# Performance work log

Measured on AMD Instinct MI355X. Metric: run time of the kernel, lower is better.

## Reference

```python
import jax, jax.numpy as jnp
import numpy as np

NUM_NODES = 1_000_000
H, OUT, R, B = 128, 64, 64, 8
N0, N1, N2 = 262144, 16384, 1024
E0, E1 = 409600, 20480


def setup_inputs() -> dict:
    key = jax.random.key(0)
    ks = jax.random.split(key, 16)
    return {
        'src_ids': jax.random.randint(ks[0], (N0,), 0, NUM_NODES, dtype=jnp.int32),
        'e0_src':  jax.random.randint(ks[1], (E0,), 0, N0, dtype=jnp.int32),
        'e0_dst':  jax.random.randint(ks[2], (E0,), 0, N1, dtype=jnp.int32),
        'e0_type': jax.random.randint(ks[3], (E0,), 0, R, dtype=jnp.int32),
        'norm0':   jax.random.uniform(ks[4], (E0,), dtype=jnp.float32),
        'e1_src':  jax.random.randint(ks[5], (E1,), 0, N1, dtype=jnp.int32),
        'e1_dst':  jax.random.randint(ks[6], (E1,), 0, N2, dtype=jnp.int32),
        'e1_type': jax.random.randint(ks[7], (E1,), 0, R, dtype=jnp.int32),
        'norm1':   jax.random.uniform(ks[8], (E1,), dtype=jnp.float32),
        'emb':   jax.random.normal(ks[9], (NUM_NODES, H), dtype=jnp.float32) * 0.02,
        'V1':    jax.random.normal(ks[10], (B, H, H), dtype=jnp.float32) / np.float32(np.sqrt(H)),
        'comp1': jax.random.normal(ks[11], (R, B), dtype=jnp.float32) / np.float32(np.sqrt(B)),
        'b1':    jnp.zeros((H,), jnp.float32),
        'V2':    jax.random.normal(ks[12], (B, H, OUT), dtype=jnp.float32) / np.float32(np.sqrt(H)),
        'comp2': jax.random.normal(ks[13], (R, B), dtype=jnp.float32) / np.float32(np.sqrt(B)),
        'b2':    jnp.zeros((OUT,), jnp.float32),
    }


def rel_graph_conv(x, src, dst, etype, norm, V, comp, bias, n_dst):
    """Basis-decomposed relational graph conv (no self loop).

    W_r = sum_b comp[r, b] * V[b];  m_e = (x[src_e] @ W_{etype_e}) * norm_e
    out[v] = sum_{e: dst_e = v} m_e + bias
    """
    h_src = x[src]                              # [E, in] gather
    c = comp[etype]                             # [E, B] per-edge basis coeffs
    m = jnp.zeros((h_src.shape[0], V.shape[2]), x.dtype)
    for b in range(V.shape[0]):                 # small fixed loop over bases
        m = m + c[:, b:b + 1] * (h_src @ V[b])  # [E, out]
    m = m * norm[:, None]
    out = jax.ops.segment_sum(m, dst, num_segments=n_dst)  # scatter-add
    return out + bias


def reference(src_ids, e0_src, e0_dst, e0_type, norm0,
              e1_src, e1_dst, e1_type, norm1,
              emb, V1, comp1, b1, V2, comp2, b2):
    x = emb[src_ids]                                                   # [N0, H] embedding lookup
    h = jax.nn.relu(rel_graph_conv(x, e0_src, e0_dst, e0_type, norm0,
                                   V1, comp1, b1, N1))                 # [N1, H]
    out = rel_graph_conv(h, e1_src, e1_dst, e1_type, norm1,
                         V2, comp2, b2, N2)                            # [N2, OUT]
    return out
```

## Files before the change

kernel.cpp:

```cpp
#include <hip/hip_runtime.h>

#define N0 262144
#define N1 16384
#define N2 1024
#define E0 409600
#define E1 20480
#define HD 128
#define PACK1 131072
#define PACK2 65536
#define BCAP 64
#define PREP_BLOCKS 2448

typedef __attribute__((ext_vector_type(8))) __bf16 bf16x8;
typedef __attribute__((ext_vector_type(4))) float f32x4;

__device__ __forceinline__ unsigned short f2bf(float f) {
    unsigned int u = __builtin_bit_cast(unsigned int, f);
    u += 0x7fffu + ((u >> 16) & 1u);
    return (unsigned short)(u >> 16);
}
__device__ __forceinline__ float bf2f(unsigned short h) {
    unsigned int u = ((unsigned int)h) << 16;
    return __builtin_bit_cast(float, u);
}

__global__ __launch_bounds__(256) void prep_k(const float* __restrict__ V1,
                                              unsigned short* __restrict__ V1p,
                                              const float* __restrict__ V2,
                                              unsigned short* __restrict__ V2p,
                                              const int* __restrict__ src_ids,
                                              const int* __restrict__ e0s,
                                              const int* __restrict__ e0d,
                                              const int* __restrict__ e0t,
                                              const float* __restrict__ n0,
                                              int* __restrict__ cnt0,
                                              int2* __restrict__ rec0,
                                              const int* __restrict__ e1s,
                                              const int* __restrict__ e1d,
                                              const int* __restrict__ e1t,
                                              const float* __restrict__ n1,
                                              int* __restrict__ cnt1,
                                              int2* __restrict__ rec1) {
    int idx = blockIdx.x * 256 + threadIdx.x;
    if (idx < PACK1 + PACK2) {
        const float* V = idx < PACK1 ? V1 : V2;
        unsigned short* o = idx < PACK1 ? V1p : V2p;
        int NT = idx < PACK1 ? 8 : 4;
        int q = idx < PACK1 ? idx : idx - PACK1;
        int i  = q & 7;
        int l  = (q >> 3) & 63;
        int kt = (q >> 9) & 31;
        int nt = q >> 14;
        int k = kt * 32 + (l >> 4) * 8 + i;
        int j = nt * 16 + (l & 15);
        o[q] = f2bf(V[(size_t)k * (NT * 16) + j]);
    } else if (idx < PACK1 + PACK2 + E0) {
        int e = idx - (PACK1 + PACK2);
        int d = e0d[e];
        int slot = atomicAdd(&cnt0[d], 1);
        if (slot < BCAP)
            rec0[(size_t)d * BCAP + slot] =
                make_int2(src_ids[e0s[e]] | (e0t[e] << 24),
                          __builtin_bit_cast(int, n0[e]));
    } else {
        int e = idx - (PACK1 + PACK2 + E0);
        int d = e1d[e];
        int slot = atomicAdd(&cnt1[d], 1);
        if (slot < BCAP)
            rec1[(size_t)d * BCAP + slot] =
                make_int2(e1s[e] | (e1t[e] << 24),
                          __builtin_bit_cast(int, n1[e]));
    }
}

template <bool L0>
__device__ __forceinline__ void agg_bucket8(const int2* __restrict__ bucket, int n,
                                            const float* __restrict__ compS,
                                            const float* __restrict__ xf,
                                            const unsigned short* __restrict__ xh,
                                            int lane, float* acc) {
#pragma unroll
    for (int i = 0; i < 16; i++) acc[i] = 0.f;
    if (n <= 0) return;
    const int last = n - 1;

    auto ldx = [&](int2 r) -> float2 {
        int s = r.x & 0xFFFFFF;
        if constexpr (L0) {
            return *(const float2*)(xf + (size_t)s * HD + lane * 2);
        } else {
            unsigned int u = *(const unsigned int*)(xh + (size_t)s * HD + lane * 2);
            return make_float2(bf2f((unsigned short)(u & 0xffffu)),
                               bf2f((unsigned short)(u >> 16)));
        }
    };
    auto consume = [&](int2 r, float2 x, bool valid) {
        float nrm = valid ? __builtin_bit_cast(float, r.y) : 0.f;
        const float* cp = compS + ((unsigned)r.x >> 24) * 8;
        float4 c0 = *(const float4*)cp;
        float4 c1 = *(const float4*)(cp + 4);
        float xx = x.x * nrm, xy = x.y * nrm;
        acc[0]  += c0.x * xx; acc[1]  += c0.x * xy;
        acc[2]  += c0.y * xx; acc[3]  += c0.y * xy;
        acc[4]  += c0.z * xx; acc[5]  += c0.z * xy;
        acc[6]  += c0.w * xx; acc[7]  += c0.w * xy;
        acc[8]  += c1.x * xx; acc[9]  += c1.x * xy;
        acc[10] += c1.y * xx; acc[11] += c1.y * xy;
        acc[12] += c1.z * xx; acc[13] += c1.z * xy;
        acc[14] += c1.w * xx; acc[15] += c1.w * xy;
    };

    for (int e = 0; e <= last; e += 8) {
        int2 r0 = bucket[e];
        int2 r1 = bucket[e + 1 <= last ? e + 1 : last];
        int2 r2 = bucket[e + 2 <= last ? e + 2 : last];
        int2 r3 = bucket[e + 3 <= last ? e + 3 : last];
        int2 r4 = bucket[e + 4 <= last ? e + 4 : last];
        int2 r5 = bucket[e + 5 <= last ? e + 5 : last];
        int2 r6 = bucket[e + 6 <= last ? e + 6 : last];
        int2 r7 = bucket[e + 7 <= last ? e + 7 : last];
        float2 x0 = ldx(r0);
        float2 x1 = ldx(r1);
        float2 x2 = ldx(r2);
        float2 x3 = ldx(r3);
        float2 x4 = ldx(r4);
        float2 x5 = ldx(r5);
        float2 x6 = ldx(r6);
        float2 x7 = ldx(r7);
        consume(r0, x0, true);
        consume(r1, x1, e + 1 <= last);
        consume(r2, x2, e + 2 <= last);
        consume(r3, x3, e + 3 <= last);
        consume(r4, x4, e + 4 <= last);
        consume(r5, x5, e + 5 <= last);
        consume(r6, x6, e + 6 <= last);
        consume(r7, x7, e + 7 <= last);
    }
}

__device__ __forceinline__ void write_lds_row(unsigned short* aT, int v, int lane,
                                              const float* acc) {
#pragma unroll
    for (int b = 0; b < 8; b++) {
        unsigned int o = (unsigned int)f2bf(acc[2 * b]) | ((unsigned int)f2bf(acc[2 * b + 1]) << 16);
        int chunk = b * 16 + (lane >> 2);
        int swc = chunk ^ (v & 15);
        *(unsigned int*)((char*)aT + (size_t)v * 2048 + swc * 16 + (lane & 3) * 4) = o;
    }
}

__global__ __launch_bounds__(512) void fused0_k(const int* __restrict__ cnt,
                                                const int2* __restrict__ rec,
                                                const float* __restrict__ comp,
                                                const float* __restrict__ emb,
                                                const unsigned short* __restrict__ Bp,
                                                const float* __restrict__ bias,
                                                unsigned short* __restrict__ hbf) {
    __shared__ unsigned short aT[16 * 1024];
    __shared__ float compS[512];
    const int t = threadIdx.x;
    const int w = t >> 6, lane = t & 63;
    const int row0 = blockIdx.x * 16;
    compS[t] = comp[t];
    __syncthreads();
    float acc[16];
    int va = row0 + w * 2;
    int na = min(cnt[va], BCAP);
    agg_bucket8<true>(rec + (size_t)va * BCAP, na, compS, emb, nullptr, lane, acc);
    write_lds_row(aT, w * 2, lane, acc);
    int vb = va + 1;
    int nb = min(cnt[vb], BCAP);
    agg_bucket8<true>(rec + (size_t)vb * BCAP, nb, compS, emb, nullptr, lane, acc);
    write_lds_row(aT, w * 2 + 1, lane, acc);
    __syncthreads();
    const int rl = lane & 15, g = lane >> 4;
    f32x4 c0 = (f32x4){0.f, 0.f, 0.f, 0.f};
#pragma unroll 4
    for (int kidx = 0; kidx < 32; kidx++) {
        bf16x8 bfr = *(const bf16x8*)(Bp + (((size_t)w * 32 + kidx) * 64 + lane) * 8);
        int ch = kidx * 4 + g;
        bf16x8 a0 = *(const bf16x8*)((const char*)aT + (size_t)rl * 2048 + (size_t)((ch ^ rl) * 16));
        c0 = __builtin_amdgcn_mfma_f32_16x16x32_bf16(a0, bfr, c0, 0, 0, 0);
    }
    int col = w * 16 + rl;
    float bv = bias[col];
#pragma unroll
    for (int q = 0; q < 4; q++) {
        int r0 = row0 + g * 4 + q;
        float v0 = c0[q] + bv;
        v0 = v0 > 0.f ? v0 : 0.f;
        hbf[(size_t)r0 * 128 + col] = f2bf(v0);
    }
}

__global__ __launch_bounds__(512) void fused1_k(const int* __restrict__ cnt,
                                                const int2* __restrict__ rec,
                                                const float* __restrict__ comp,
                                                const unsigned short* __restrict__ hbf,
                                                const unsigned short* __restrict__ Bp,
                                                const float* __restrict__ bias,
                                                float* __restrict__ out) {
    __shared__ unsigned short aT[16 * 1024];
    __shared__ f32x4 red[8 * 64];
    __shared__ float compS[512];
    const int t = threadIdx.x;
    const int w = t >> 6, lane = t & 63;
    const int row0 = blockIdx.x * 16;
    compS[t] = comp[t];
    __syncthreads();
    float acc[16];
    int va = row0 + w * 2;
    int na = min(cnt[va], BCAP);
    agg_bucket8<false>(rec + (size_t)va * BCAP, na, compS, nullptr, hbf, lane, acc);
    write_lds_row(aT, w * 2, lane, acc);
    int vb = va + 1;
    int nb = min(cnt[vb], BCAP);
    agg_bucket8<false>(rec + (size_t)vb * BCAP, nb, compS, nullptr, hbf, lane, acc);
    write_lds_row(aT, w * 2 + 1, lane, acc);
    __syncthreads();
    const int kh = w >> 2, nt = w & 3;
    const int rl = lane & 15, g = lane >> 4;
    f32x4 c = (f32x4){0.f, 0.f, 0.f, 0.f};
#pragma unroll 4
    for (int k = 0; k < 16; k++) {
        int kidx = kh * 16 + k;
        bf16x8 bfr = *(const bf16x8*)(Bp + (((size_t)nt * 32 + kidx) * 64 + lane) * 8);
        int ch = kidx * 4 + g;
        bf16x8 a0 = *(const bf16x8*)((const char*)aT + (size_t)rl * 2048 + (size_t)((ch ^ rl) * 16));
        c = __builtin_amdgcn_mfma_f32_16x16x32_bf16(a0, bfr, c, 0, 0, 0);
    }
    red[w * 64 + lane] = c;
    __syncthreads();
    if (w < 4) {
        f32x4 a = red[w * 64 + lane];
        f32x4 b = red[(w + 4) * 64 + lane];
        int col = nt * 16 + rl;
        float bv = bias[col];
#pragma unroll
        for (int q = 0; q < 4; q++) {
            int r0 = row0 + g * 4 + q;
            out[(size_t)r0 * 64 + col] = a[q] + b[q] + bv;
        }
    }
}

extern "C" void kernel_launch(void* const* d_in, const int* in_sizes, int n_in,
                              void* d_out, int out_size, void* d_ws, size_t ws_size,
                              hipStream_t stream) {
    const int*   src_ids = (const int*)d_in[0];
    const int*   e0_src  = (const int*)d_in[1];
    const int*   e0_dst  = (const int*)d_in[2];
    const int*   e0_type = (const int*)d_in[3];
    const float* norm0   = (const float*)d_in[4];
    const int*   e1_src  = (const int*)d_in[5];
    const int*   e1_dst  = (const int*)d_in[6];
    const int*   e1_type = (const int*)d_in[7];
    const float* norm1   = (const float*)d_in[8];
    const float* emb     = (const float*)d_in[9];
    const float* V1      = (const float*)d_in[10];
    const float* comp1   = (const float*)d_in[11];
    const float* b1      = (const float*)d_in[12];
    const float* V2      = (const float*)d_in[13];
    const float* comp2   = (const float*)d_in[14];
    const float* b2      = (const float*)d_in[15];
    float* out = (float*)d_out;

    char* base = (char*)d_ws;
    size_t off = 0;
    auto alloc = [&](size_t bytes) -> char* {
        off = (off + 255) & ~(size_t)255;
        char* r = base + off;
        off += bytes;
        return r;
    };
    unsigned short* hbf = (unsigned short*)alloc((size_t)N1 * HD * 2);
    unsigned short* V1p = (unsigned short*)alloc((size_t)1024 * 128 * 2);
    unsigned short* V2p = (unsigned short*)alloc((size_t)1024 * 64 * 2);
    int*   cnt    = (int*)alloc((size_t)(N1 + N2) * 4);
    int*   cnt0   = cnt;
    int*   cnt1   = cnt + N1;
    int2*  rec0   = (int2*)alloc((size_t)N1 * BCAP * 8);
    int2*  rec1   = (int2*)alloc((size_t)N2 * BCAP * 8);
    (void)ws_size; (void)in_sizes; (void)n_in; (void)out_size;

    hipMemsetAsync(cnt, 0, (size_t)(N1 + N2) * 4, stream);

    prep_k<<<PREP_BLOCKS, 256, 0, stream>>>(V1, V1p, V2, V2p,
                                            src_ids, e0_src, e0_dst, e0_type, norm0,
                                            cnt0, rec0,
                                            e1_src, e1_dst, e1_type, norm1,
                                            cnt1, rec1);
    fused0_k<<<N1 / 16, 512, 0, stream>>>(cnt0, rec0, comp1, emb, V1p, b1, hbf);
    fused1_k<<<N2 / 16, 512, 0, stream>>>(cnt1, rec1, comp2, hbf, V2p, b2, out);
}
```

Baseline: 93.32 us.

## Stream edge records and embedding rows into LDS with double-buffered async loads

Replaces the layer-0 per-destination gather loop with a software pipeline. Each wave first copies its bucket records into LDS using global_load_lds. It then issues async direct-to-LDS loads of embedding rows, four edges per stage, over two buffers, so gathers for the next stage overlap the basis-coefficient accumulation of the current one. The aim is to hide embedding gather latency. In exchange it uses more LDS, which may reduce occupancy, and the manual vmcnt waits are fragile.

```diff
diff --git a/kernel.cpp b/kernel.cpp
--- a/kernel.cpp
+++ b/kernel.cpp
@@ -13,6 +13,10 @@
 
 typedef __attribute__((ext_vector_type(8))) __bf16 bf16x8;
 typedef __attribute__((ext_vector_type(4))) float f32x4;
+
+#define GLD4(g, l) __builtin_amdgcn_global_load_lds(                        \
+    (const __attribute__((address_space(1))) void*)(g),                     \
+    (__attribute__((address_space(3))) void*)(l), 4, 0, 0)
 
 __device__ __forceinline__ unsigned short f2bf(float f) {
     unsigned int u = __builtin_bit_cast(unsigned int, f);
@@ -158,20 +162,84 @@
                                                 unsigned short* __restrict__ hbf) {
     __shared__ unsigned short aT[16 * 1024];
     __shared__ float compS[512];
+    __shared__ int2  ldsRec[8][128];
+    __shared__ float ldsX[8][2][4][HD];
     const int t = threadIdx.x;
     const int w = t >> 6, lane = t & 63;
     const int row0 = blockIdx.x * 16;
     compS[t] = comp[t];
     __syncthreads();
+
+    const int va = row0 + w * 2;
+    const int na = min(cnt[va], BCAP);
+    const int nb = min(cnt[va + 1], BCAP);
+
+    {
+        const float* gr = (const float*)(rec + (size_t)va * BCAP);
+        float* lr = (float*)ldsRec[w];
+#pragma unroll
+        for (int j = 0; j < 4; j++)
+            GLD4(gr + j * 64 + lane, lr + j * 64);
+        asm volatile("s_waitcnt vmcnt(0)" ::: "memory");
+        __builtin_amdgcn_sched_barrier(0);
+    }
+
     float acc[16];
-    int va = row0 + w * 2;
-    int na = min(cnt[va], BCAP);
-    agg_bucket8<true>(rec + (size_t)va * BCAP, na, compS, emb, nullptr, lane, acc);
-    write_lds_row(aT, w * 2, lane, acc);
-    int vb = va + 1;
-    int nb = min(cnt[vb], BCAP);
-    agg_bucket8<true>(rec + (size_t)vb * BCAP, nb, compS, emb, nullptr, lane, acc);
-    write_lds_row(aT, w * 2 + 1, lane, acc);
+#pragma unroll
+    for (int bi = 0; bi < 2; bi++) {
+        const int n = bi ? nb : na;
+        const int2* recB = ldsRec[w] + bi * 64;
+#pragma unroll
+        for (int i = 0; i < 16; i++) acc[i] = 0.f;
+        if (n > 0) {
+            auto issue = [&](int c, int s) {
+#pragma unroll
+                for (int r = 0; r < 4; r++) {
+                    int e = c * 4 + r;
+                    e = e <= n - 1 ? e : n - 1;
+                    int src = recB[e].x & 0xFFFFFF;
+                    const float* g = emb + (size_t)src * HD + lane;
+                    float* l = &ldsX[w][s][r][0];
+                    GLD4(g, l);
+                    GLD4(g + 64, l + 64);
+                }
+            };
+            auto consume = [&](int c, int s) {
+#pragma unroll
+                for (int r = 0; r < 4; r++) {
+                    int e0 = c * 4 + r;
+                    bool valid = e0 < n;
+                    int e = valid ? e0 : n - 1;
+                    int2 rc = recB[e];
+                    float nrm = valid ? __builtin_bit_cast(float, rc.y) : 0.f;
+                    const float* cp = compS + ((unsigned)rc.x >> 24) * 8;
+                    float4 c0 = *(const float4*)cp;
+                    float4 c1 = *(const float4*)(cp + 4);
+                    float2 x = *(const float2*)&ldsX[w][s][r][lane * 2];
+                    float xx = x.x * nrm, xy = x.y * nrm;
+                    acc[0]  += c0.x * xx; acc[1]  += c0.x * xy;
+                    acc[2]  += c0.y * xx; acc[3]  += c0.y * xy;
+                    acc[4]  += c0.z * xx; acc[5]  += c0.z * xy;
+                    acc[6]  += c0.w * xx; acc[7]  += c0.w * xy;
+                    acc[8]  += c1.x * xx; acc[9]  += c1.x * xy;
+                    acc[10] += c1.y * xx; acc[11] += c1.y * xy;
+                    acc[12] += c1.z * xx; acc[13] += c1.z * xy;
+                    acc[14] += c1.w * xx; acc[15] += c1.w * xy;
+                }
+            };
+            const int nc = (n + 3) >> 2;
+            issue(0, 0);
+            issue(1, 1);
+            for (int c = 0; c < nc; c++) {
+                if (c + 1 < nc) { asm volatile("s_waitcnt vmcnt(8)" ::: "memory"); }
+                else            { asm volatile("s_waitcnt vmcnt(0)" ::: "memory"); }
+                __builtin_amdgcn_sched_barrier(0);
+                consume(c, c & 1);
+                if (c + 2 < nc) issue(c + 2, c & 1);
+            }
+        }
+        write_lds_row(aT, w * 2 + bi, lane, acc);
+    }
     __syncthreads();
     const int rl = lane & 15, g = lane >> 4;
     f32x4 c0 = (f32x4){0.f, 0.f, 0.f, 0.f};
```

Result: faster. 91.42 us (-2.0%).

## Aggregate each destination row block-wide via LDS staging instead of per-warp buckets

Applied to the files above, without the earlier changes.

Replaces the per-wavefront bucket aggregation (each wave handling two destination rows) with a block-cooperative loop over the 16 rows. For each row, the block stages per-edge basis coefficients and the gathered source embeddings in LDS as bf16, then each thread reduces one basis/channel pair over the edges. The aim is to spread the gather across all waves and balance uneven edge counts. It adds two block barriers per row (32 per block), a serial edge loop per thread, and bf16 rounding of the inputs before accumulation.

```diff
diff --git a/kernel.cpp b/kernel.cpp
--- a/kernel.cpp
+++ b/kernel.cpp
@@ -157,22 +157,73 @@
                                                 const float* __restrict__ bias,
                                                 unsigned short* __restrict__ hbf) {
     __shared__ unsigned short aT[16 * 1024];
+    __shared__ unsigned short xB[64 * 128];
+    __shared__ unsigned short cA[1024];
     __shared__ float compS[512];
     const int t = threadIdx.x;
     const int w = t >> 6, lane = t & 63;
     const int row0 = blockIdx.x * 16;
     compS[t] = comp[t];
     __syncthreads();
-    float acc[16];
-    int va = row0 + w * 2;
-    int na = min(cnt[va], BCAP);
-    agg_bucket8<true>(rec + (size_t)va * BCAP, na, compS, emb, nullptr, lane, acc);
-    write_lds_row(aT, w * 2, lane, acc);
-    int vb = va + 1;
-    int nb = min(cnt[vb], BCAP);
-    agg_bucket8<true>(rec + (size_t)vb * BCAP, nb, compS, emb, nullptr, lane, acc);
-    write_lds_row(aT, w * 2 + 1, lane, acc);
-    __syncthreads();
+
+    const int bb = t >> 6;
+    const int chg = t & 63;
+
+    for (int s = 0; s < 16; s++) {
+        const int v = row0 + s;
+        const int n = min(cnt[v], BCAP);
+        const int2* recV = rec + (size_t)v * BCAP;
+        __syncthreads();
+
+        {
+            const int b = t & 15;
+            const int k0 = t >> 4;
+#pragma unroll
+            for (int j = 0; j < 2; j++) {
+                int k = j * 32 + k0;
+                unsigned short cv = 0;
+                if (b < 8 && k < n) {
+                    int2 rc = recV[k];
+                    float nrm = __builtin_bit_cast(float, rc.y);
+                    cv = f2bf(compS[((unsigned)rc.x >> 24) * 8 + b] * nrm);
+                }
+                cA[((k >> 3) * 16 + b) * 8 + (k & 7)] = cv;
+            }
+        }
+#pragma unroll
+        for (int j = 0; j < 8; j++) {
+            int k = w * 8 + j;
+            if (k < n) {
+                int src = recV[k].x & 0xFFFFFF;
+                float2 xv = *(const float2*)(emb + (size_t)src * HD + lane * 2);
+                int ch = lane * 2;
+                int base = (k >> 3) * 128;
+                int kl = k & 7;
+                xB[(base + ch) * 8 + kl]     = f2bf(xv.x);
+                xB[(base + ch + 1) * 8 + kl] = f2bf(xv.y);
+            }
+        }
+        __syncthreads();
+
+        float a0 = 0.f, a1 = 0.f;
+        for (int k = 0; k < n; k++) {
+            float cv = bf2f(cA[((k >> 3) * 16 + bb) * 8 + (k & 7)]);
+            float x0 = bf2f(xB[((k >> 3) * 128 + chg) * 8 + (k & 7)]);
+            float x1 = bf2f(xB[((k >> 3) * 128 + chg + 64) * 8 + (k & 7)]);
+            a0 += cv * x0;
+            a1 += cv * x1;
+        }
+        {
+            int kk0 = bb * 128 + chg;
+            *(unsigned short*)((char*)aT + s * 2048 +
+                (((kk0 >> 3) ^ s) * 16) + (kk0 & 7) * 2) = f2bf(a0);
+            int kk1 = kk0 + 64;
+            *(unsigned short*)((char*)aT + s * 2048 +
+                (((kk1 >> 3) ^ s) * 16) + (kk1 & 7) * 2) = f2bf(a1);
+        }
+    }
+    __syncthreads();
+
     const int rl = lane & 15, g = lane >> 4;
     f32x4 c0 = (f32x4){0.f, 0.f, 0.f, 0.f};
 #pragma unroll 4
```

After: 236.8 us. 154% more time.
